# Performance work log

Hardware: AMD Instinct MI355X
Metric: run time of the kernel (lower is better)

Reference implementation:

```python
import jax, jax.numpy as jnp
import numpy as np
import math

B = 32; N = 512000; D = 64; NENT = 100000; NEDGE = 1000000; NREL = 200
K_SOURCE = 100; K_MIN = 50; K_MAX = 1000; L_INFL = 4; A_SLOPE = 1.0
TEMP = 1.0; LAM_NOISE = 1.0; COS_EPS = 1e-8


def compute_topk(l):
    # sigmoid schedule for layer-dependent Top-K (python ints, trace-time)
    if l < L_INFL:
        s = 1.0 / (1.0 + math.exp(-A_SLOPE * (l - L_INFL / 2)))
        return int(K_SOURCE + (K_MAX - K_SOURCE) * s)
    s = 1.0 / (1.0 + math.exp(-A_SLOPE * (l - 3 * L_INFL / 2)))
    return int(K_MIN + (K_MAX - K_MIN) * (1.0 - s))


def setup_inputs():
    key = jax.random.key(0)
    k = jax.random.split(key, 14)
    i = jnp.arange(N)
    b = i % B                     # batches interleaved -> every batch has diff nodes
    e = (i // B) * 6 + b          # unique entity per (batch, node), max < NENT
    nodes = jnp.stack([b, e], axis=1)
    return {
        "hidden": jax.random.normal(k[0], (N, D), jnp.float32),
        "nodes": nodes,
        "scores": jax.random.uniform(k[1], (N,), jnp.float32) + 0.1,
        "h0": jax.random.normal(k[2], (1, N, D), jnp.float32),
        "alpha": jax.random.normal(k[3], (NEDGE, 1), jnp.float32),
        "hidden_q": jax.random.normal(k[4], (B, D), jnp.float32),
        "q_rel": jax.random.randint(k[5], (B,), 0, 2 * NREL + 1),
        "edges": jax.random.randint(k[6], (NEDGE, 6), 0, N),
        "old_nodes_new_idx": jnp.arange(N // 2),
        "batch_size": B,
        "message": jax.random.normal(k[7], (NEDGE, D), jnp.float32),
        "obj": jax.random.randint(k[8], (NEDGE,), 0, N),
        "alpha_temp": jax.random.normal(k[9], (NEDGE, 1), jnp.float32),
        "l": 2,
        "noise": jax.random.normal(k[10], (N, 3), jnp.float32),
        "mlp_w1": jax.random.normal(k[11], (2 * D, D), jnp.float32) * 0.05,
        "mlp_b1": jnp.zeros((D,), jnp.float32),
        "mlp_w2": jax.random.normal(k[12], (D, D), jnp.float32) * 0.05,
        "mlp_b2": jnp.zeros((D,), jnp.float32),
        "rel_embed": jax.random.normal(k[13], (2 * NREL + 1, D), jnp.float32) * 0.05,
        "expert_emb": jax.random.normal(jax.random.fold_in(key, 1), (3, D), jnp.float32),
        "w_n": jax.random.normal(jax.random.fold_in(key, 2), (D,), jnp.float32) * 0.05,
    }


def _dense_topk_mult(vals, bidx, eidx, diff, K, B_):
    # scatter per-diff-node values into dense [B, n_ent], softmax over entities,
    # top-K hard mask, straight-through multiplier (hard - sg(p) + p) on diff nodes.
    neg = jnp.float32(-jnp.inf)
    dense = jnp.full((B_, NENT), neg, jnp.float32).at[bidx, eidx].set(jnp.where(diff, vals, neg))
    probs = jax.nn.softmax(dense, axis=1)
    _, idx = jax.lax.top_k(probs, K)
    hard = jnp.zeros((B_, NENT), bool).at[jnp.arange(B_)[:, None], idx].set(True)
    p = probs[bidx, eidx]
    h = hard[bidx, eidx].astype(jnp.float32)
    return jnp.where(diff, h - jax.lax.stop_gradient(p) + p, 1.0)


def _forward(hidden, scores, h0, hidden_q, alpha_temp, mlp_w1, mlp_b1, mlp_w2, mlp_b2,
             rel_embed, expert_emb, w_n, nodes, q_rel, edges, old_nodes_new_idx,
             batch_size, noise, l):
    bidx = nodes[:, 0]
    eidx = nodes[:, 1]
    # ---- noisy gate over 3 pruning experts ----
    q_rel_e = rel_embed[q_rel]                                   # [B, D]
    ctx_in = jnp.concatenate([hidden_q[bidx], q_rel_e[bidx]], axis=-1)  # [N, 2D]
    ctx = jax.nn.relu(ctx_in @ mlp_w1 + mlp_b1) @ mlp_w2 + mlp_b2       # [N, D]
    escore = ctx @ expert_emb.T                                  # [N, 3]
    nscale = jax.nn.softplus(ctx @ w_n)[:, None]                 # [N, 1]
    escore = escore + LAM_NOISE * noise * nscale
    weights = jax.nn.softmax(escore / TEMP, axis=-1)             # [N, 3]
    importance = weights.sum(0) / weights.sum()                  # [3], sums to 1
    w = importance  # num_pruning_experts=3: topk over all 3 + renorm is identity

    diff = jnp.ones((N,), bool).at[old_nodes_new_idx].set(False)
    K_l = compute_topk(l)

    # expert 0: score-based pruner
    m0 = _dense_topk_mult(scores, bidx, eidx, diff, K_l, batch_size)

    # expert 1: cosine-similarity pruner (hidden vs query relation embedding)
    qn = q_rel_e[bidx]
    num = (hidden * qn).sum(-1)
    den = jnp.maximum(jnp.linalg.norm(hidden, axis=-1), COS_EPS) * \
          jnp.maximum(jnp.linalg.norm(qn, axis=-1), COS_EPS)
    m1 = _dense_topk_mult(num / den, bidx, eidx, diff, K_l, batch_size)

    # expert 2: alpha pruner -- segment-max of edge attention onto target nodes,
    # softmax over the global node dim, top-K among new nodes only.
    obj_e = edges[:, 5]
    mx = jax.ops.segment_max(alpha_temp[:, 0], obj_e, num_segments=N)
    node_probs = jax.nn.softmax(mx / TEMP)
    masked = jnp.where(diff, node_probs, -1.0)   # probs >= 0, so topk lands on diff
    _, top_i = jax.lax.top_k(masked, K_l)
    hard2 = jnp.zeros((N,), bool).at[top_i].set(True)
    m2 = jnp.where(diff, hard2.astype(jnp.float32) - jax.lax.stop_gradient(node_probs) + node_probs, 1.0)

    # ---- combine: each expert returns the full node set with diff rows rescaled,
    # and the hashed node-id lookup is the identity permutation here, so the
    # index_add combine reduces to a weighted sum of multipliers. ----
    wm = w[0] * m0 + w[1] * m1 + w[2] * m2                        # [N]
    hidden_c = hidden * wm[:, None]
    scores_c = scores * wm
    h0_c = h0 * wm[None, :, None]

    cv = jnp.std(weights, ddof=1) / (weights.mean() + 1e-5)       # torch unbiased std
    L_imp = cv ** 2
    return hidden_c, scores_c, h0_c, L_imp


def reference(hidden, nodes, scores, h0, alpha, hidden_q, q_rel, edges,
              old_nodes_new_idx, batch_size, message, obj, alpha_temp, l, noise,
              mlp_w1, mlp_b1, mlp_w2, mlp_b2, rel_embed, expert_emb, w_n):
    # alpha / message / obj are passed through in the original but unused in the
    # computed path; the final scores!=0 row filter is replaced by keeping the
    # full (zero-preserving) arrays to stay jit-compatible.
    return _forward(hidden, scores, h0, hidden_q, alpha_temp, mlp_w1, mlp_b1,
                    mlp_w2, mlp_b2, rel_embed, expert_emb, w_n, nodes, q_rel,
                    edges, old_nodes_new_idx, batch_size, noise, l)
```

## Files before the change

### kernel.cpp

```cpp
#include <hip/hip_runtime.h>
#include <stdint.h>
#include <math.h>

#define DD 64
#define K_SOURCE_C 100
#define K_MIN_C 50
#define K_MAX_C 1000
#define L_INFL_C 4
#define A_SLOPE_C 1.0
#define COS_EPS_C 1e-8f
#define NBINS 8192
#define CAPC 3584
#define NHB 192
#define NWB 1024

__device__ __forceinline__ uint32_t f2mono(float f) {
    uint32_t u = __float_as_uint(f);
    return (u & 0x80000000u) ? ~u : (u | 0x80000000u);
}

__constant__ int c_shifts[5] = {51, 38, 25, 12, 0};
__constant__ int c_nbits[5]  = {13, 13, 13, 13, 12};

__global__ void init_kernel(uint32_t* mx, uint8_t* diff, int* cnt,
                            int* Kp, int* node_cnt, uint32_t* ghist,
                            const int* l_ptr, int N, int B) {
    int i = blockIdx.x * blockDim.x + threadIdx.x;
    if (i < N) { mx[i] = 0u; diff[i] = 1; }
    if (i < B) cnt[i] = 0;
    if (i < NBINS) ghist[i] = 0u;
    if (i == 0) {
        *node_cnt = 0;
        double l = (double)(*l_ptr);
        int K;
        if (l < (double)L_INFL_C) {
            double s = 1.0 / (1.0 + exp(-A_SLOPE_C * (l - L_INFL_C / 2.0)));
            K = (int)(K_SOURCE_C + (K_MAX_C - K_SOURCE_C) * s);
        } else {
            double s = 1.0 / (1.0 + exp(-A_SLOPE_C * (l - 3.0 * L_INFL_C / 2.0)));
            K = (int)(K_MIN_C + (K_MAX_C - K_MIN_C) * (1.0 - s));
        }
        *Kp = K;
    }
}

__global__ void diff_kernel(uint8_t* diff, const int* old_idx, int n_old, int N) {
    int j = blockIdx.x * blockDim.x + threadIdx.x;
    if (j < n_old) { int idx = old_idx[j]; if (idx >= 0 && idx < N) diff[idx] = 0; }
}

__global__ void ctx_kernel(const float* hidden_q, const int* q_rel, const float* rel_embed,
                           const float* w1, const float* b1, const float* w2, const float* b2,
                           const float* expert_emb, const float* w_n,
                           float* escore, float* nscale, float* qvec, float* qnorm, int B) {
    int b = blockIdx.x, t = threadIdx.x;
    __shared__ float cin[2 * DD];
    __shared__ float h1s[DD];
    int q = q_rel[b];
    float qv = rel_embed[(size_t)q * DD + t];
    qvec[b * DD + t] = qv;
    cin[t] = hidden_q[b * DD + t];
    cin[DD + t] = qv;
    __syncthreads();
    float acc = b1[t];
    for (int j = 0; j < 2 * DD; j++) acc += cin[j] * w1[j * DD + t];
    h1s[t] = fmaxf(acc, 0.f);
    __syncthreads();
    float c = b2[t];
    for (int j = 0; j < DD; j++) c += h1s[j] * w2[j * DD + t];
    float e0 = c * expert_emb[0 * DD + t];
    float e1 = c * expert_emb[1 * DD + t];
    float e2 = c * expert_emb[2 * DD + t];
    float wn = c * w_n[t];
    float qq = qv * qv;
    for (int m = 32; m >= 1; m >>= 1) {
        e0 += __shfl_xor(e0, m); e1 += __shfl_xor(e1, m); e2 += __shfl_xor(e2, m);
        wn += __shfl_xor(wn, m); qq += __shfl_xor(qq, m);
    }
    if (t == 0) {
        escore[b * 3 + 0] = e0; escore[b * 3 + 1] = e1; escore[b * 3 + 2] = e2;
        nscale[b] = fmaxf(wn, 0.f) + log1pf(expf(-fabsf(wn)));
        qnorm[b] = fmaxf(sqrtf(qq), COS_EPS_C);
    }
}

__global__ void segmax_kernel(const int* edges, const float* alpha_temp, uint32_t* mx,
                              int NE, int N) {
    int e = blockIdx.x * blockDim.x + threadIdx.x;
    if (e < NE) {
        int o = edges[(size_t)e * 6 + 5];
        if (o >= 0 && o < N) atomicMax(&mx[o], f2mono(alpha_temp[e]));
    }
}

__global__ void nodewc_kernel(const float* hidden, const int* nodes, const float* noise,
                              const float* qvec, const float* qnorm,
                              const float* escore, const float* nscale,
                              float* cosvals, double* partials, int N, int B) {
    int t = threadIdx.x;
    int sub = t & 15;
    double s0 = 0, s1 = 0, s2 = 0, sq = 0;
    int ngroups = (N + 15) >> 4;
    for (int g = blockIdx.x; g < ngroups; g += gridDim.x) {
        int node = g * 16 + (t >> 4);
        if (node < N) {
            int b = nodes[2 * node];
            bool bv = (b >= 0 && b < B);
            float4 h4 = *(const float4*)(hidden + (size_t)node * DD + sub * 4);
            float num = 0.f;
            if (bv) {
                float4 q4 = *(const float4*)(qvec + b * DD + sub * 4);
                num = h4.x * q4.x + h4.y * q4.y + h4.z * q4.z + h4.w * q4.w;
            }
            float hs = h4.x * h4.x + h4.y * h4.y + h4.z * h4.z + h4.w * h4.w;
            for (int m = 8; m >= 1; m >>= 1) { num += __shfl_xor(num, m); hs += __shfl_xor(hs, m); }
            if (sub == 0) {
                float qn = bv ? qnorm[b] : COS_EPS_C;
                cosvals[node] = num / (fmaxf(sqrtf(hs), COS_EPS_C) * qn);
                if (bv) {
                    float ns = nscale[b];
                    float e0 = escore[b * 3 + 0] + noise[3 * node + 0] * ns;
                    float e1 = escore[b * 3 + 1] + noise[3 * node + 1] * ns;
                    float e2 = escore[b * 3 + 2] + noise[3 * node + 2] * ns;
                    float mm = fmaxf(e0, fmaxf(e1, e2));
                    float x0 = expf(e0 - mm), x1 = expf(e1 - mm), x2 = expf(e2 - mm);
                    float s = x0 + x1 + x2;
                    x0 /= s; x1 /= s; x2 /= s;
                    s0 += x0; s1 += x1; s2 += x2;
                    sq += (double)x0 * x0 + (double)x1 * x1 + (double)x2 * x2;
                }
            }
        }
    }
    for (int m = 32; m >= 1; m >>= 1) {
        s0 += __shfl_xor(s0, m); s1 += __shfl_xor(s1, m);
        s2 += __shfl_xor(s2, m); sq += __shfl_xor(sq, m);
    }
    __shared__ double red[4][4];
    int wid = t >> 6, lane = t & 63;
    if (lane == 0) { red[wid][0] = s0; red[wid][1] = s1; red[wid][2] = s2; red[wid][3] = sq; }
    __syncthreads();
    if (t == 0) {
        double a0 = 0, a1 = 0, a2 = 0, a3 = 0;
        for (int w = 0; w < 4; w++) { a0 += red[w][0]; a1 += red[w][1]; a2 += red[w][2]; a3 += red[w][3]; }
        partials[blockIdx.x * 4 + 0] = a0;
        partials[blockIdx.x * 4 + 1] = a1;
        partials[blockIdx.x * 4 + 2] = a2;
        partials[blockIdx.x * 4 + 3] = a3;
    }
}

__global__ void stats_kernel(const double* partials, float* wvec, float* out_L, int N) {
    int t = threadIdx.x;
    double s0 = 0, s1 = 0, s2 = 0, sq = 0;
    for (int i = t; i < NWB; i += 256) {
        s0 += partials[4 * i + 0]; s1 += partials[4 * i + 1];
        s2 += partials[4 * i + 2]; sq += partials[4 * i + 3];
    }
    for (int m = 32; m >= 1; m >>= 1) {
        s0 += __shfl_xor(s0, m); s1 += __shfl_xor(s1, m);
        s2 += __shfl_xor(s2, m); sq += __shfl_xor(sq, m);
    }
    __shared__ double red[4][4];
    int wid = t >> 6, lane = t & 63;
    if (lane == 0) { red[wid][0] = s0; red[wid][1] = s1; red[wid][2] = s2; red[wid][3] = sq; }
    __syncthreads();
    if (t == 0) {
        double c0 = 0, c1 = 0, c2 = 0, S2 = 0;
        for (int w = 0; w < 4; w++) { c0 += red[w][0]; c1 += red[w][1]; c2 += red[w][2]; S2 += red[w][3]; }
        double tot = c0 + c1 + c2;
        wvec[0] = (float)(c0 / tot); wvec[1] = (float)(c1 / tot); wvec[2] = (float)(c2 / tot);
        double n = 3.0 * (double)N;
        double mean = tot / n;
        double var = (S2 - tot * tot / n) / (n - 1.0);
        if (var < 0) var = 0;
        double cv = sqrt(var) / (mean + 1e-5);
        *out_L = (float)(cv * cv);
    }
}

__global__ void compact_kernel(const int* nodes, const uint8_t* diff, const float* scores,
                               const float* cosvals, const uint32_t* mx,
                               uint64_t* keys0, uint64_t* keys1, uint64_t* nkeys,
                               int* cnt, int* node_cnt, int N, int B, int CAP) {
    __shared__ int lcnt[64];
    __shared__ int lbase[64];
    __shared__ int nloc_cnt, nloc_base;
    int t = threadIdx.x;
    if (t < B) lcnt[t] = 0;
    if (t == 0) nloc_cnt = 0;
    __syncthreads();
    int i = blockIdx.x * blockDim.x + t;
    int b = -1, loc = 0, nl = 0;
    bool isdiff = (i < N) && diff[i];
    if (isdiff) {
        nl = atomicAdd(&nloc_cnt, 1);
        int bb = nodes[2 * i];
        if (bb >= 0 && bb < B) { b = bb; loc = atomicAdd(&lcnt[b], 1); }
    }
    __syncthreads();
    if (t < B) lbase[t] = lcnt[t] ? atomicAdd(&cnt[t], lcnt[t]) : 0;
    if (t == 0) nloc_base = nloc_cnt ? atomicAdd(node_cnt, nloc_cnt) : 0;
    __syncthreads();
    if (isdiff) {
        nkeys[nloc_base + nl] = ((uint64_t)mx[i] << 32) | (uint64_t)(0xFFFFFFFFu - (uint32_t)i);
        if (b >= 0) {
            int pos = lbase[b] + loc;
            if (pos < CAP) {
                int ei = nodes[2 * i + 1];
                uint64_t tb = (uint64_t)(0xFFFFFFFFu - (uint32_t)ei);
                keys0[(size_t)b * CAP + pos] = ((uint64_t)f2mono(scores[i]) << 32) | tb;
                keys1[(size_t)b * CAP + pos] = ((uint64_t)f2mono(cosvals[i]) << 32) | tb;
            }
        }
    }
}

struct PickScratch { uint32_t wtot[16]; int fd; uint32_t fK; uint32_t total; };

__device__ void block_pick(const uint32_t* hist, int nbins, uint32_t Kr, PickScratch* sc) {
    int t = threadIdx.x;
    int PB = nbins >> 10;
    int lane = t & 63, wid = t >> 6;
    uint32_t csum = 0;
    for (int j = 0; j < PB; j++) csum += hist[PB * t + j];
    uint32_t ssum = csum;
    for (int off = 1; off < 64; off <<= 1) {
        uint32_t v = __shfl_down(ssum, off, 64);
        if (lane + off < 64) ssum += v;
    }
    if (lane == 0) sc->wtot[wid] = ssum;
    if (t == 0) sc->fd = -1;
    __syncthreads();
    uint32_t above = 0, total = 0;
    for (int w = 0; w < 16; w++) {
        uint32_t v = sc->wtot[w];
        total += v;
        if (w > wid) above += v;
    }
    uint32_t gcnt = ssum + above - csum;
    int fd = -1; uint32_t fK = 0;
    for (int j = PB - 1; j >= 0; j--) {
        uint32_t h = hist[PB * t + j];
        if (h && gcnt < Kr && gcnt + h >= Kr) { fd = PB * t + j; fK = Kr - gcnt; }
        gcnt += h;
    }
    if (fd >= 0) { sc->fd = fd; sc->fK = fK; }
    if (t == 0) sc->total = total;
    __syncthreads();
}

__global__ __launch_bounds__(1024)
void selA_kernel(const uint64_t* keys0, const uint64_t* keys1, const int* cnt,
                 const uint64_t* nkeys, const int* node_cnt, uint32_t* ghist,
                 uint64_t* T, const int* Kp, int B, int CAP) {
    __shared__ uint32_t hist[NBINS];
    __shared__ PickScratch sc;
    int t = threadIdx.x;
    int blk = blockIdx.x;
    if (blk < 2 * B) {
        int row = (blk < B) ? blk : blk - B;
        const uint64_t* list = ((blk < B) ? keys0 : keys1) + (size_t)row * CAP;
        int n = min(cnt[row], CAP);
        int K = *Kp;
        if (n <= K) { if (t == 0) T[blk] = 0ull; return; }
        uint64_t pref = 0ull;
        uint32_t Kr = (uint32_t)K;
        for (int lev = 0; lev < 5; lev++) {
            int nb = 1 << c_nbits[lev];
            for (int j = t; j < nb; j += 1024) hist[j] = 0;
            __syncthreads();
            uint64_t pmask = (lev == 0) ? 0ull : (~0ull << c_shifts[lev - 1]);
            int sh = c_shifts[lev];
            uint32_t bmask = (uint32_t)(nb - 1);
            for (int i = t; i < n; i += 1024) {
                uint64_t key = list[i];
                if ((key & pmask) == pref)
                    atomicAdd(&hist[(uint32_t)(key >> sh) & bmask], 1u);
            }
            __syncthreads();
            block_pick(hist, nb, Kr, &sc);
            if (sc.fd < 0) { if (t == 0) T[blk] = 0ull; return; }
            pref |= ((uint64_t)sc.fd) << sh;
            Kr = sc.fK;
            __syncthreads();
        }
        if (t == 0) T[blk] = pref;
    } else {
        int nb = blk - 2 * B;
        for (int j = t; j < NBINS; j += 1024) hist[j] = 0;
        __syncthreads();
        int n = *node_cnt;
        for (int i = nb * 1024 + t; i < n; i += NHB * 1024)
            atomicAdd(&hist[(uint32_t)(nkeys[i] >> 51)], 1u);
        __syncthreads();
        for (int j = t; j < NBINS; j += 1024) {
            uint32_t v = hist[j];
            if (v) atomicAdd(&ghist[j], v);
        }
    }
}

__global__ __launch_bounds__(1024)
void selB_kernel(const uint64_t* nkeys, const int* node_cnt, const uint32_t* ghist,
                 uint64_t* T, const int* Kp, int B) {
    __shared__ uint32_t hist[NBINS];
    __shared__ uint64_t cand[CAPC];
    __shared__ PickScratch sc;
    __shared__ int ccnt;
    int t = threadIdx.x;
    int K = *Kp;
    int n = *node_cnt;
    for (int j = t; j < NBINS; j += 1024) hist[j] = ghist[j];
    __syncthreads();
    block_pick(hist, NBINS, (uint32_t)K, &sc);
    if (sc.total <= (uint32_t)K || sc.fd < 0) { if (t == 0) T[2 * B] = 0ull; return; }
    int fd0 = sc.fd;
    uint64_t pref = ((uint64_t)fd0) << 51;
    uint32_t Kr = sc.fK;
    if (t == 0) ccnt = 0;
    __syncthreads();
    for (int i = t; i < n; i += 1024) {
        uint64_t key = nkeys[i];
        if ((int)(key >> 51) == fd0) {
            int p = atomicAdd(&ccnt, 1);
            if (p < CAPC) cand[p] = key;
        }
    }
    __syncthreads();
    int m = ccnt;
    bool inlds = (m <= CAPC);
    if (!inlds) m = n;
    for (int lev = 1; lev < 5; lev++) {
        int nb = 1 << c_nbits[lev];
        for (int j = t; j < nb; j += 1024) hist[j] = 0;
        __syncthreads();
        uint64_t pmask = ~0ull << c_shifts[lev - 1];
        int sh = c_shifts[lev];
        uint32_t bmask = (uint32_t)(nb - 1);
        for (int i = t; i < m; i += 1024) {
            uint64_t key = inlds ? cand[i] : nkeys[i];
            if ((key & pmask) == pref)
                atomicAdd(&hist[(uint32_t)(key >> sh) & bmask], 1u);
        }
        __syncthreads();
        block_pick(hist, nb, Kr, &sc);
        if (sc.fd < 0) { if (t == 0) T[2 * B] = 0ull; return; }
        pref |= ((uint64_t)sc.fd) << sh;
        Kr = sc.fK;
        __syncthreads();
    }
    if (t == 0) T[2 * B] = pref;
}

__global__ void final_kernel(const float* hidden, const float* h0, const float* scores,
                             const int* nodes, const uint8_t* diff, const float* cosvals,
                             const uint32_t* mx, const uint64_t* T, const float* wvec,
                             float* out_hidden, float* out_scores, float* out_h0,
                             int N, int B) {
    int t = threadIdx.x;
    int node = blockIdx.x * 16 + (t >> 4);
    int sub = t & 15;
    if (node >= N) return;
    float w0 = wvec[0], w1 = wvec[1], w2 = wvec[2];
    float wm;
    if (!diff[node]) {
        wm = w0 + w1 + w2;
    } else {
        int b = nodes[2 * node];
        int ei = nodes[2 * node + 1];
        float m0 = 0.f, m1 = 0.f;
        if (b >= 0 && b < B) {
            uint64_t tb = (uint64_t)(0xFFFFFFFFu - (uint32_t)ei);
            uint64_t k0 = ((uint64_t)f2mono(scores[node]) << 32) | tb;
            uint64_t k1 = ((uint64_t)f2mono(cosvals[node]) << 32) | tb;
            m0 = (k0 >= T[b]) ? 1.f : 0.f;
            m1 = (k1 >= T[B + b]) ? 1.f : 0.f;
        }
        uint64_t k2 = ((uint64_t)mx[node] << 32) | (uint64_t)(0xFFFFFFFFu - (uint32_t)node);
        float m2 = (k2 >= T[2 * B]) ? 1.f : 0.f;
        wm = w0 * m0 + w1 * m1 + w2 * m2;
    }
    size_t off = (size_t)node * DD + sub * 4;
    float4 h4 = *(const float4*)(hidden + off);
    float4 g4 = *(const float4*)(h0 + off);
    float4 o1, o2;
    o1.x = h4.x * wm; o1.y = h4.y * wm; o1.z = h4.z * wm; o1.w = h4.w * wm;
    o2.x = g4.x * wm; o2.y = g4.y * wm; o2.z = g4.z * wm; o2.w = g4.w * wm;
    *(float4*)(out_hidden + off) = o1;
    *(float4*)(out_h0 + off) = o2;
    if (sub == 0) out_scores[node] = scores[node] * wm;
}

extern "C" void kernel_launch(void* const* d_in, const int* in_sizes, int n_in,
                              void* d_out, int out_size, void* d_ws, size_t ws_size,
                              hipStream_t stream) {
    const float* hidden     = (const float*)d_in[0];
    const int*   nodes      = (const int*)d_in[1];
    const float* scores     = (const float*)d_in[2];
    const float* h0         = (const float*)d_in[3];
    const float* hidden_q   = (const float*)d_in[5];
    const int*   q_rel      = (const int*)d_in[6];
    const int*   edges      = (const int*)d_in[7];
    const int*   old_idx    = (const int*)d_in[8];
    const float* alpha_temp = (const float*)d_in[12];
    const int*   l_ptr      = (const int*)d_in[13];
    const float* noise      = (const float*)d_in[14];
    const float* mw1        = (const float*)d_in[15];
    const float* mb1        = (const float*)d_in[16];
    const float* mw2        = (const float*)d_in[17];
    const float* mb2        = (const float*)d_in[18];
    const float* rel_embed  = (const float*)d_in[19];
    const float* expert_emb = (const float*)d_in[20];
    const float* w_n        = (const float*)d_in[21];

    int N     = in_sizes[2];
    int NE    = in_sizes[12];
    int n_old = in_sizes[8];
    int B     = in_sizes[5] / DD;
    int CAP   = N / B;
    int nsel  = 2 * B + 1;

    size_t off = 0;
    auto take = [&](size_t bytes) -> size_t {
        size_t p = off; off += (bytes + 15) & ~(size_t)15; return p;
    };
    char* wsb = (char*)d_ws;
    float*    cosvals  = (float*)   (wsb + take((size_t)N * 4));
    uint32_t* mx       = (uint32_t*)(wsb + take((size_t)N * 4));
    uint8_t*  diff     = (uint8_t*) (wsb + take((size_t)N));
    int*      cnt      = (int*)     (wsb + take((size_t)B * 4));
    double*   partials = (double*)  (wsb + take((size_t)NWB * 4 * 8));
    int*      Kp       = (int*)     (wsb + take(16));
    int*      node_cnt = (int*)     (wsb + take(16));
    float*    escore   = (float*)   (wsb + take((size_t)B * 3 * 4));
    float*    nscale   = (float*)   (wsb + take((size_t)B * 4));
    float*    qvec     = (float*)   (wsb + take((size_t)B * DD * 4));
    float*    qnorm    = (float*)   (wsb + take((size_t)B * 4));
    float*    wvec     = (float*)   (wsb + take(16));
    uint64_t* T        = (uint64_t*)(wsb + take((size_t)nsel * 8));
    uint32_t* ghist    = (uint32_t*)(wsb + take((size_t)NBINS * 4));
    size_t keys_bytes  = (size_t)B * CAP * 8;
    size_t nkeys_bytes = (size_t)N * 8;
    uint64_t *keys0, *keys1, *nkeys;
    if (ws_size >= off + 2 * keys_bytes + nkeys_bytes) {
        keys0 = (uint64_t*)(wsb + take(keys_bytes));
        keys1 = (uint64_t*)(wsb + take(keys_bytes));
        nkeys = (uint64_t*)(wsb + take(nkeys_bytes));
    } else {
        keys0 = (uint64_t*)d_out;
        keys1 = keys0 + (size_t)B * CAP;
        nkeys = keys1 + (size_t)B * CAP;
    }

    float* out_hidden = (float*)d_out;
    float* out_scores = out_hidden + (size_t)N * DD;
    float* out_h0     = out_scores + N;
    float* out_L      = out_h0 + (size_t)N * DD;

    int nb = (N + 255) / 256;
    init_kernel<<<nb, 256, 0, stream>>>(mx, diff, cnt, Kp, node_cnt, ghist, l_ptr, N, B);
    diff_kernel<<<(n_old + 255) / 256, 256, 0, stream>>>(diff, old_idx, n_old, N);
    ctx_kernel<<<B, 64, 0, stream>>>(hidden_q, q_rel, rel_embed, mw1, mb1, mw2, mb2,
                                     expert_emb, w_n, escore, nscale, qvec, qnorm, B);
    segmax_kernel<<<(NE + 255) / 256, 256, 0, stream>>>(edges, alpha_temp, mx, NE, N);
    nodewc_kernel<<<NWB, 256, 0, stream>>>(hidden, nodes, noise, qvec, qnorm,
                                           escore, nscale, cosvals, partials, N, B);
    stats_kernel<<<1, 256, 0, stream>>>(partials, wvec, out_L, N);
    compact_kernel<<<nb, 256, 0, stream>>>(nodes, diff, scores, cosvals, mx,
                                           keys0, keys1, nkeys, cnt, node_cnt, N, B, CAP);
    selA_kernel<<<2 * B + NHB, 1024, 0, stream>>>(keys0, keys1, cnt, nkeys, node_cnt,
                                                  ghist, T, Kp, B, CAP);
    selB_kernel<<<1, 1024, 0, stream>>>(nkeys, node_cnt, ghist, T, Kp, B);
    final_kernel<<<(N + 15) / 16, 256, 0, stream>>>(hidden, h0, scores, nodes, diff, cosvals,
                                                    mx, T, wvec, out_hidden, out_scores, out_h0, N, B);
}
```

Before: 833.0 us.

## Fuse all pipeline stages into one cooperative persistent kernel with grid syncs

Replaces the sequence of ten kernel launches with a single cooperative kernel of 1024 blocks that runs every stage (init, ctx MLP, segmax, cosine/gating stats, compaction, per-batch radix select, global select, final scaling) and separates them with grid-wide syncs. The global top-K selection now gathers candidates whose top digit matches into a small buffer before refining, instead of rescanning all node keys in one block. Launch overhead and inter-kernel gaps are removed, at the cost of grid-sync latency, fixed occupancy (launch bounds 256x4), and single-block serial phases holding the whole grid idle. The old multi-kernel path is kept as a fallback if the cooperative launch fails.

```diff
diff --git a/kernel.cpp b/kernel.cpp
--- a/kernel.cpp
+++ b/kernel.cpp
@@ -1,6 +1,9 @@
 #include <hip/hip_runtime.h>
+#include <hip/hip_cooperative_groups.h>
 #include <stdint.h>
 #include <math.h>
+
+namespace cg = cooperative_groups;
 
 #define DD 64
 #define K_SOURCE_C 100
@@ -13,6 +16,8 @@
 #define CAPC 3584
 #define NHB 192
 #define NWB 1024
+#define GBLK 1024
+#define CAPG 65536
 
 __device__ __forceinline__ uint32_t f2mono(float f) {
     uint32_t u = __float_as_uint(f);
@@ -21,6 +26,383 @@
 
 __constant__ int c_shifts[5] = {51, 38, 25, 12, 0};
 __constant__ int c_nbits[5]  = {13, 13, 13, 13, 12};
+
+
+struct FusedParams {
+    const float *hidden, *scores, *h0, *hidden_q, *alpha_temp, *noise;
+    const float *mw1, *mb1, *mw2, *mb2, *rel_embed, *expert_emb, *w_n;
+    const int *nodes, *q_rel, *edges, *old_idx, *l_ptr;
+    float *cosvals; uint32_t *mx; uint8_t *diff; int *cnt; double *partials;
+    int *Kp; int *node_cnt; float *escore, *nscale, *qvec, *qnorm, *wvec;
+    uint64_t *T; uint32_t *ghist; uint64_t *gcand; int *gccnt; uint32_t *g_state;
+    uint64_t *keys0, *keys1, *nkeys;
+    float *out_hidden, *out_scores, *out_h0, *out_L;
+    int N, NE, n_old, B, CAP;
+};
+
+struct PickScratch4 { uint32_t wtot[4]; int fd; uint32_t fK; uint32_t total; };
+
+__device__ void block_pick256(const uint32_t* hist, int nbins, uint32_t Kr, PickScratch4* sc) {
+    int t = threadIdx.x;
+    int PB = nbins >> 8;
+    int lane = t & 63, wid = t >> 6;
+    uint32_t csum = 0;
+    for (int j = 0; j < PB; j++) csum += hist[PB * t + j];
+    uint32_t ssum = csum;
+    for (int off = 1; off < 64; off <<= 1) {
+        uint32_t v = __shfl_down(ssum, off, 64);
+        if (lane + off < 64) ssum += v;
+    }
+    if (lane == 0) sc->wtot[wid] = ssum;
+    if (t == 0) sc->fd = -1;
+    __syncthreads();
+    uint32_t above = 0, total = 0;
+    for (int w = 0; w < 4; w++) {
+        uint32_t v = sc->wtot[w];
+        total += v;
+        if (w > wid) above += v;
+    }
+    uint32_t gcnt = ssum + above - csum;
+    int fd = -1; uint32_t fK = 0;
+    for (int j = PB - 1; j >= 0; j--) {
+        uint32_t h = hist[PB * t + j];
+        if (h && gcnt < Kr && gcnt + h >= Kr) { fd = PB * t + j; fK = Kr - gcnt; }
+        gcnt += h;
+    }
+    if (fd >= 0) { sc->fd = fd; sc->fK = fK; }
+    if (t == 0) sc->total = total;
+    __syncthreads();
+}
+
+union ShMem {
+    uint32_t hist[NBINS];
+    struct { float cin[2 * DD]; float h1s[DD]; } ctx;
+    double red[4][4];
+    struct { int lcnt[64]; int lbase[64]; } cp;
+};
+
+__global__ __launch_bounds__(256, 4)
+void fused_kernel(FusedParams p) {
+    cg::grid_group grid = cg::this_grid();
+    __shared__ ShMem sh;
+    __shared__ PickScratch4 sc;
+    __shared__ int s_nloc[2];
+    int t = threadIdx.x, blk = blockIdx.x, G = gridDim.x;
+
+    for (int i = blk * 256 + t; i < p.N; i += G * 256) { p.mx[i] = 0u; p.diff[i] = 1; }
+    for (int i = blk * 256 + t; i < NBINS; i += G * 256) p.ghist[i] = 0u;
+    if (blk == 0 && t < p.B) p.cnt[t] = 0;
+    if (blk == 0 && t == 0) {
+        *p.node_cnt = 0; *p.gccnt = 0;
+        double l = (double)(*p.l_ptr);
+        int K;
+        if (l < (double)L_INFL_C) {
+            double s = 1.0 / (1.0 + exp(-A_SLOPE_C * (l - L_INFL_C / 2.0)));
+            K = (int)(K_SOURCE_C + (K_MAX_C - K_SOURCE_C) * s);
+        } else {
+            double s = 1.0 / (1.0 + exp(-A_SLOPE_C * (l - 3.0 * L_INFL_C / 2.0)));
+            K = (int)(K_MIN_C + (K_MAX_C - K_MIN_C) * (1.0 - s));
+        }
+        *p.Kp = K;
+    }
+    if (blk < p.B) {
+        int b = blk;
+        float qv = 0.f;
+        if (t < DD) {
+            int q = p.q_rel[b];
+            qv = p.rel_embed[(size_t)q * DD + t];
+            p.qvec[b * DD + t] = qv;
+            sh.ctx.cin[t] = p.hidden_q[b * DD + t];
+            sh.ctx.cin[DD + t] = qv;
+        }
+        __syncthreads();
+        if (t < DD) {
+            float acc = p.mb1[t];
+            for (int j = 0; j < 2 * DD; j++) acc += sh.ctx.cin[j] * p.mw1[j * DD + t];
+            sh.ctx.h1s[t] = fmaxf(acc, 0.f);
+        }
+        __syncthreads();
+        if (t < DD) {
+            float c = p.mb2[t];
+            for (int j = 0; j < DD; j++) c += sh.ctx.h1s[j] * p.mw2[j * DD + t];
+            float e0 = c * p.expert_emb[0 * DD + t];
+            float e1 = c * p.expert_emb[1 * DD + t];
+            float e2 = c * p.expert_emb[2 * DD + t];
+            float wn = c * p.w_n[t];
+            float qq = qv * qv;
+            for (int m = 32; m >= 1; m >>= 1) {
+                e0 += __shfl_xor(e0, m); e1 += __shfl_xor(e1, m); e2 += __shfl_xor(e2, m);
+                wn += __shfl_xor(wn, m); qq += __shfl_xor(qq, m);
+            }
+            if (t == 0) {
+                p.escore[b * 3 + 0] = e0; p.escore[b * 3 + 1] = e1; p.escore[b * 3 + 2] = e2;
+                p.nscale[b] = fmaxf(wn, 0.f) + log1pf(expf(-fabsf(wn)));
+                p.qnorm[b] = fmaxf(sqrtf(qq), COS_EPS_C);
+            }
+        }
+    }
+    grid.sync();
+
+    for (int j = blk * 256 + t; j < p.n_old; j += G * 256) {
+        int idx = p.old_idx[j];
+        if (idx >= 0 && idx < p.N) p.diff[idx] = 0;
+    }
+    for (int e = blk * 256 + t; e < p.NE; e += G * 256) {
+        int o = p.edges[(size_t)e * 6 + 5];
+        if (o >= 0 && o < p.N) atomicMax(&p.mx[o], f2mono(p.alpha_temp[e]));
+    }
+    grid.sync();
+
+    {
+        int sub = t & 15;
+        double s0 = 0, s1 = 0, s2 = 0, sq = 0;
+        int ngroups = (p.N + 15) >> 4;
+        for (int g = blk; g < ngroups; g += G) {
+            int node = g * 16 + (t >> 4);
+            if (node < p.N) {
+                int b = p.nodes[2 * node];
+                bool bv = (b >= 0 && b < p.B);
+                float4 h4 = *(const float4*)(p.hidden + (size_t)node * DD + sub * 4);
+                float num = 0.f;
+                if (bv) {
+                    float4 q4 = *(const float4*)(p.qvec + b * DD + sub * 4);
+                    num = h4.x * q4.x + h4.y * q4.y + h4.z * q4.z + h4.w * q4.w;
+                }
+                float hs = h4.x * h4.x + h4.y * h4.y + h4.z * h4.z + h4.w * h4.w;
+                for (int m = 8; m >= 1; m >>= 1) { num += __shfl_xor(num, m); hs += __shfl_xor(hs, m); }
+                if (sub == 0) {
+                    float qn = bv ? p.qnorm[b] : COS_EPS_C;
+                    p.cosvals[node] = num / (fmaxf(sqrtf(hs), COS_EPS_C) * qn);
+                    if (bv) {
+                        float ns = p.nscale[b];
+                        float e0 = p.escore[b * 3 + 0] + p.noise[3 * node + 0] * ns;
+                        float e1 = p.escore[b * 3 + 1] + p.noise[3 * node + 1] * ns;
+                        float e2 = p.escore[b * 3 + 2] + p.noise[3 * node + 2] * ns;
+                        float mm = fmaxf(e0, fmaxf(e1, e2));
+                        float x0 = expf(e0 - mm), x1 = expf(e1 - mm), x2 = expf(e2 - mm);
+                        float s = x0 + x1 + x2;
+                        x0 /= s; x1 /= s; x2 /= s;
+                        s0 += x0; s1 += x1; s2 += x2;
+                        sq += (double)x0 * x0 + (double)x1 * x1 + (double)x2 * x2;
+                    }
+                }
+            }
+        }
+        for (int m = 32; m >= 1; m >>= 1) {
+            s0 += __shfl_xor(s0, m); s1 += __shfl_xor(s1, m);
+            s2 += __shfl_xor(s2, m); sq += __shfl_xor(sq, m);
+        }
+        int wid = t >> 6, lane = t & 63;
+        if (lane == 0) { sh.red[wid][0] = s0; sh.red[wid][1] = s1; sh.red[wid][2] = s2; sh.red[wid][3] = sq; }
+        __syncthreads();
+        if (t == 0) {
+            double a0 = 0, a1 = 0, a2 = 0, a3 = 0;
+            for (int w = 0; w < 4; w++) { a0 += sh.red[w][0]; a1 += sh.red[w][1]; a2 += sh.red[w][2]; a3 += sh.red[w][3]; }
+            p.partials[blk * 4 + 0] = a0; p.partials[blk * 4 + 1] = a1;
+            p.partials[blk * 4 + 2] = a2; p.partials[blk * 4 + 3] = a3;
+        }
+    }
+    grid.sync();
+
+    for (int i0 = blk * 256; i0 < p.N; i0 += G * 256) {
+        if (t < p.B) sh.cp.lcnt[t] = 0;
+        if (t == 0) s_nloc[0] = 0;
+        __syncthreads();
+        int i = i0 + t;
+        int b = -1, loc = 0, nl = 0;
+        bool isdiff = (i < p.N) && p.diff[i];
+        if (isdiff) {
+            nl = atomicAdd(&s_nloc[0], 1);
+            int bb = p.nodes[2 * i];
+            if (bb >= 0 && bb < p.B) { b = bb; loc = atomicAdd(&sh.cp.lcnt[b], 1); }
+        }
+        __syncthreads();
+        if (t < p.B) sh.cp.lbase[t] = sh.cp.lcnt[t] ? atomicAdd(&p.cnt[t], sh.cp.lcnt[t]) : 0;
+        if (t == 0) s_nloc[1] = s_nloc[0] ? atomicAdd(p.node_cnt, s_nloc[0]) : 0;
+        __syncthreads();
+        if (isdiff) {
+            p.nkeys[s_nloc[1] + nl] = ((uint64_t)p.mx[i] << 32) | (uint64_t)(0xFFFFFFFFu - (uint32_t)i);
+            if (b >= 0) {
+                int pos = sh.cp.lbase[b] + loc;
+                if (pos < p.CAP) {
+                    int ei = p.nodes[2 * i + 1];
+                    uint64_t tb = (uint64_t)(0xFFFFFFFFu - (uint32_t)ei);
+                    p.keys0[(size_t)b * p.CAP + pos] = ((uint64_t)f2mono(p.scores[i]) << 32) | tb;
+                    p.keys1[(size_t)b * p.CAP + pos] = ((uint64_t)f2mono(p.cosvals[i]) << 32) | tb;
+                }
+            }
+        }
+        __syncthreads();
+    }
+    grid.sync();
+
+    if (blk < 2 * p.B) {
+        int row = (blk < p.B) ? blk : blk - p.B;
+        const uint64_t* list = ((blk < p.B) ? p.keys0 : p.keys1) + (size_t)row * p.CAP;
+        int n = min(p.cnt[row], p.CAP);
+        int K = *p.Kp;
+        if (n <= K) {
+            if (t == 0) p.T[blk] = 0ull;
+        } else {
+            uint64_t pref = 0ull; uint32_t Kr = (uint32_t)K; bool ok = true;
+            for (int lev = 0; lev < 5 && ok; lev++) {
+                int nb2 = 1 << c_nbits[lev];
+                for (int j = t; j < nb2; j += 256) sh.hist[j] = 0;
+                __syncthreads();
+                uint64_t pmask = (lev == 0) ? 0ull : (~0ull << c_shifts[lev - 1]);
+                int shf = c_shifts[lev];
+                uint32_t bmask = (uint32_t)(nb2 - 1);
+                for (int i = t; i < n; i += 256) {
+                    uint64_t key = list[i];
+                    if ((key & pmask) == pref)
+                        atomicAdd(&sh.hist[(uint32_t)(key >> shf) & bmask], 1u);
+                }
+                __syncthreads();
+                block_pick256(sh.hist, nb2, Kr, &sc);
+                if (sc.fd < 0) ok = false;
+                else { pref |= ((uint64_t)sc.fd) << shf; Kr = sc.fK; }
+                __syncthreads();
+            }
+            if (t == 0) p.T[blk] = ok ? pref : 0ull;
+        }
+    } else {
+        for (int j = t; j < NBINS; j += 256) sh.hist[j] = 0;
+        __syncthreads();
+        int n = *p.node_cnt;
+        int base = (blk - 2 * p.B) * 256 + t;
+        int stride = (G - 2 * p.B) * 256;
+        for (int i = base; i < n; i += stride)
+            atomicAdd(&sh.hist[(uint32_t)(p.nkeys[i] >> 51)], 1u);
+        __syncthreads();
+        for (int j = t; j < NBINS; j += 256) {
+            uint32_t v = sh.hist[j];
+            if (v) atomicAdd(&p.ghist[j], v);
+        }
+    }
+    grid.sync();
+
+    if (blk == 0) {
+        int K = *p.Kp;
+        block_pick256(p.ghist, NBINS, (uint32_t)K, &sc);
+        if (t == 0) {
+            if (sc.total <= (uint32_t)K || sc.fd < 0) { p.T[2 * p.B] = 0ull; p.g_state[0] = 0xFFFFFFFFu; }
+            else { p.g_state[0] = (uint32_t)sc.fd; p.g_state[1] = sc.fK; }
+        }
+        double s0 = 0, s1 = 0, s2 = 0, sq = 0;
+        for (int i = t; i < G; i += 256) {
+            s0 += p.partials[4 * i + 0]; s1 += p.partials[4 * i + 1];
+            s2 += p.partials[4 * i + 2]; sq += p.partials[4 * i + 3];
+        }
+        for (int m = 32; m >= 1; m >>= 1) {
+            s0 += __shfl_xor(s0, m); s1 += __shfl_xor(s1, m);
+            s2 += __shfl_xor(s2, m); sq += __shfl_xor(sq, m);
+        }
+        int wid = t >> 6, lane = t & 63;
+        __syncthreads();
+        if (lane == 0) { sh.red[wid][0] = s0; sh.red[wid][1] = s1; sh.red[wid][2] = s2; sh.red[wid][3] = sq; }
+        __syncthreads();
+        if (t == 0) {
+            double c0 = 0, c1 = 0, c2 = 0, S2 = 0;
+            for (int w = 0; w < 4; w++) { c0 += sh.red[w][0]; c1 += sh.red[w][1]; c2 += sh.red[w][2]; S2 += sh.red[w][3]; }
+            double tot = c0 + c1 + c2;
+            p.wvec[0] = (float)(c0 / tot); p.wvec[1] = (float)(c1 / tot); p.wvec[2] = (float)(c2 / tot);
+            double n = 3.0 * (double)p.N;
+            double mean = tot / n;
+            double var = (S2 - tot * tot / n) / (n - 1.0);
+            if (var < 0) var = 0;
+            double cv = sqrt(var) / (mean + 1e-5);
+            *p.out_L = (float)(cv * cv);
+        }
+    }
+    grid.sync();
+
+    {
+        uint32_t fd0 = p.g_state[0];
+        if (fd0 != 0xFFFFFFFFu) {
+            int n = *p.node_cnt;
+            for (int i = blk * 256 + t; i < n; i += G * 256) {
+                uint64_t key = p.nkeys[i];
+                if ((uint32_t)(key >> 51) == fd0) {
+                    int pos = atomicAdd(p.gccnt, 1);
+                    if (pos < CAPG) p.gcand[pos] = key;
+                }
+            }
+        }
+    }
+    grid.sync();
+
+    if (blk == 0) {
+        uint32_t fd0 = p.g_state[0];
+        if (fd0 != 0xFFFFFFFFu) {
+            int tot = *p.gccnt;
+            const uint64_t* src = p.gcand;
+            int mm = tot;
+            if (tot > CAPG) { src = p.nkeys; mm = *p.node_cnt; }
+            uint64_t pref = ((uint64_t)fd0) << 51;
+            uint32_t Kr = p.g_state[1];
+            bool ok = true;
+            for (int lev = 1; lev < 5 && ok; lev++) {
+                int nb2 = 1 << c_nbits[lev];
+                for (int j = t; j < nb2; j += 256) sh.hist[j] = 0;
+                __syncthreads();
+                uint64_t pmask = ~0ull << c_shifts[lev - 1];
+                int shf = c_shifts[lev];
+                uint32_t bmask = (uint32_t)(nb2 - 1);
+                for (int i = t; i < mm; i += 256) {
+                    uint64_t key = src[i];
+                    if ((key & pmask) == pref)
+                        atomicAdd(&sh.hist[(uint32_t)(key >> shf) & bmask], 1u);
+                }
+                __syncthreads();
+                block_pick256(sh.hist, nb2, Kr, &sc);
+                if (sc.fd < 0) ok = false;
+                else { pref |= ((uint64_t)sc.fd) << shf; Kr = sc.fK; }
+                __syncthreads();
+            }
+            if (t == 0) p.T[2 * p.B] = ok ? pref : 0ull;
+        }
+    }
+    grid.sync();
+
+    {
+        float w0 = p.wvec[0], w1 = p.wvec[1], w2 = p.wvec[2];
+        int sub = t & 15;
+        int ngroups = (p.N + 15) >> 4;
+        for (int g = blk; g < ngroups; g += G) {
+            int node = g * 16 + (t >> 4);
+            if (node < p.N) {
+                float wm;
+                if (!p.diff[node]) {
+                    wm = w0 + w1 + w2;
+                } else {
+                    int b = p.nodes[2 * node];
+                    int ei = p.nodes[2 * node + 1];
+                    float m0 = 0.f, m1 = 0.f;
+                    if (b >= 0 && b < p.B) {
+                        uint64_t tb = (uint64_t)(0xFFFFFFFFu - (uint32_t)ei);
+                        uint64_t k0 = ((uint64_t)f2mono(p.scores[node]) << 32) | tb;
+                        uint64_t k1 = ((uint64_t)f2mono(p.cosvals[node]) << 32) | tb;
+                        m0 = (k0 >= p.T[b]) ? 1.f : 0.f;
+                        m1 = (k1 >= p.T[p.B + b]) ? 1.f : 0.f;
+                    }
+                    uint64_t k2 = ((uint64_t)p.mx[node] << 32) | (uint64_t)(0xFFFFFFFFu - (uint32_t)node);
+                    float m2 = (k2 >= p.T[2 * p.B]) ? 1.f : 0.f;
+                    wm = w0 * m0 + w1 * m1 + w2 * m2;
+                }
+                size_t off = (size_t)node * DD + sub * 4;
+                float4 h4 = *(const float4*)(p.hidden + off);
+                float4 g4 = *(const float4*)(p.h0 + off);
+                float4 o1, o2;
+                o1.x = h4.x * wm; o1.y = h4.y * wm; o1.z = h4.z * wm; o1.w = h4.w * wm;
+                o2.x = g4.x * wm; o2.y = g4.y * wm; o2.z = g4.z * wm; o2.w = g4.w * wm;
+                *(float4*)(p.out_hidden + off) = o1;
+                *(float4*)(p.out_h0 + off) = o2;
+                if (sub == 0) p.out_scores[node] = p.scores[node] * wm;
+            }
+        }
+    }
+}
+
 
 __global__ void init_kernel(uint32_t* mx, uint8_t* diff, int* cnt,
                             int* Kp, int* node_cnt, uint32_t* ghist,
@@ -392,6 +774,7 @@
     if (sub == 0) out_scores[node] = scores[node] * wm;
 }
 
+
 extern "C" void kernel_launch(void* const* d_in, const int* in_sizes, int n_in,
                               void* d_out, int out_size, void* d_ws, size_t ws_size,
                               hipStream_t stream) {
@@ -440,6 +823,9 @@
     float*    wvec     = (float*)   (wsb + take(16));
     uint64_t* T        = (uint64_t*)(wsb + take((size_t)nsel * 8));
     uint32_t* ghist    = (uint32_t*)(wsb + take((size_t)NBINS * 4));
+    uint64_t* gcand    = (uint64_t*)(wsb + take((size_t)CAPG * 8));
+    int*      gccnt    = (int*)     (wsb + take(16));
+    uint32_t* g_state  = (uint32_t*)(wsb + take(16));
     size_t keys_bytes  = (size_t)B * CAP * 8;
     size_t nkeys_bytes = (size_t)N * 8;
     uint64_t *keys0, *keys1, *nkeys;
@@ -457,6 +843,26 @@
     float* out_scores = out_hidden + (size_t)N * DD;
     float* out_h0     = out_scores + N;
     float* out_L      = out_h0 + (size_t)N * DD;
+
+    FusedParams fp;
+    fp.hidden = hidden; fp.scores = scores; fp.h0 = h0; fp.hidden_q = hidden_q;
+    fp.alpha_temp = alpha_temp; fp.noise = noise;
+    fp.mw1 = mw1; fp.mb1 = mb1; fp.mw2 = mw2; fp.mb2 = mb2;
+    fp.rel_embed = rel_embed; fp.expert_emb = expert_emb; fp.w_n = w_n;
+    fp.nodes = nodes; fp.q_rel = q_rel; fp.edges = edges; fp.old_idx = old_idx; fp.l_ptr = l_ptr;
+    fp.cosvals = cosvals; fp.mx = mx; fp.diff = diff; fp.cnt = cnt; fp.partials = partials;
+    fp.Kp = Kp; fp.node_cnt = node_cnt; fp.escore = escore; fp.nscale = nscale;
+    fp.qvec = qvec; fp.qnorm = qnorm; fp.wvec = wvec;
+    fp.T = T; fp.ghist = ghist; fp.gcand = gcand; fp.gccnt = gccnt; fp.g_state = g_state;
+    fp.keys0 = keys0; fp.keys1 = keys1; fp.nkeys = nkeys;
+    fp.out_hidden = out_hidden; fp.out_scores = out_scores; fp.out_h0 = out_h0; fp.out_L = out_L;
+    fp.N = N; fp.NE = NE; fp.n_old = n_old; fp.B = B; fp.CAP = CAP;
+
+    void* kargs[] = { (void*)&fp };
+    hipError_t rc = hipLaunchCooperativeKernel(fused_kernel, dim3(GBLK), dim3(256),
+                                               kargs, 0, stream);
+    if (rc == hipSuccess) return;
+    (void)hipGetLastError();
 
     int nb = (N + 255) / 256;
     init_kernel<<<nb, 256, 0, stream>>>(mx, diff, cnt, Kp, node_cnt, ghist, l_ptr, N, B);
```

Result: slower. 1.727 ms (+107.4%).
